# Performance work log

Hardware: AMD Instinct MI355X
Metric: run time of the kernel (lower is better)

Reference implementation:

```python
import jax, jax.numpy as jnp
import numpy as np

B, S, D, H = 2, 2048, 1024, 16
DH = D // H
NEG = -1000000000.0


def setup_inputs() -> dict:
    key = jax.random.key(0)
    ks = jax.random.split(key, 8)
    q = jax.random.normal(ks[0], (B, S, D), dtype=jnp.float32)
    k = jax.random.normal(ks[1], (B, S, D), dtype=jnp.float32)
    v = jax.random.normal(ks[2], (B, S, D), dtype=jnp.float32)
    # padding mask [B, k_len]; ensure first key position is valid
    mask = jax.random.randint(ks[3], (B, S), 0, 2, dtype=jnp.int32)
    mask = mask.at[:, 0].set(1)
    scale = 1.0 / np.sqrt(D)
    Wq = jax.random.normal(ks[4], (D, D), dtype=jnp.float32) * scale
    Wk = jax.random.normal(ks[5], (D, D), dtype=jnp.float32) * scale
    Wv = jax.random.normal(ks[6], (D, D), dtype=jnp.float32) * scale
    Wo = jax.random.normal(ks[7], (D, D), dtype=jnp.float32) * scale
    return {"q": q, "k": k, "v": v, "mask": mask,
            "Wq": Wq, "Wk": Wk, "Wv": Wv, "Wo": Wo}


def reference(q, k, v, mask, Wq, Wk, Wv, Wo):
    # nn.Linear(bias=False): y = x @ W.T  (W is [out, in])
    Q = jnp.einsum('bsd,ed->bse', q, Wq)
    K = jnp.einsum('bsd,ed->bse', k, Wk)
    V = jnp.einsum('bsd,ed->bse', v, Wv)
    # split heads -> [B, H, S, DH]
    Q = Q.reshape(B, S, H, DH).transpose(0, 2, 1, 3)
    K = K.reshape(B, S, H, DH).transpose(0, 2, 1, 3)
    V = V.reshape(B, S, H, DH).transpose(0, 2, 1, 3)
    scores = jnp.einsum('bhqd,bhkd->bhqk', Q, K) / jnp.float32(np.sqrt(DH))
    # padding mask: [B, K] -> additive [B, 1, 1, K]
    pad = jnp.where(mask == 0, jnp.float32(NEG), jnp.float32(0.0))[:, None, None, :]
    scores = scores + pad
    # causal (mask_future=True): strict upper triangle blocked
    causal = jnp.where(jnp.triu(jnp.ones((S, S), dtype=bool), k=1),
                       jnp.float32(NEG), jnp.float32(0.0))
    scores = scores + causal
    attn = jax.nn.softmax(scores, axis=-1)
    out = jnp.einsum('bhqk,bhkd->bhqd', attn, V)  # [B, H, S, DH]
    out = out.transpose(0, 2, 1, 3).reshape(B, S, D)
    out = jnp.einsum('bsd,ed->bse', out, Wo)
    # dropout: identity in eval mode
    return out
```

## Files before the change

### kernel.cpp

```cpp
#include <hip/hip_runtime.h>
#include <stdint.h>

#define BB 2
#define SS 2048
#define DD 1024
#define HH 16
#define DHH 64

typedef __bf16 bf16_t;
typedef bf16_t bf16x8 __attribute__((ext_vector_type(8)));
typedef float f32x4 __attribute__((ext_vector_type(4)));
typedef short s16x4 __attribute__((ext_vector_type(4)));

union FragU { uint4 u; bf16x8 b; };
union Frag4U { uint2 u; s16x4 s; };

#if __has_builtin(__builtin_amdgcn_exp2f)
#define EXP2(x) __builtin_amdgcn_exp2f(x)
#else
#define EXP2(x) exp2f(x)
#endif

__device__ __forceinline__ unsigned short f2bf(float f) {
  union { float f; unsigned int u; } x; x.f = f;
  unsigned int u = x.u;
  return (unsigned short)((u + 0x7FFFu + ((u >> 16) & 1u)) >> 16);
}

__device__ __forceinline__ uint2 pack4(float4 v) {
  uint2 r;
  r.x = (unsigned)f2bf(v.x) | ((unsigned)f2bf(v.y) << 16);
  r.y = (unsigned)f2bf(v.z) | ((unsigned)f2bf(v.w) << 16);
  return r;
}

__device__ __forceinline__ uint2 packAcc(f32x4 a) {
  uint2 r;
  r.x = (unsigned)f2bf(a[0]) | ((unsigned)f2bf(a[1]) << 16);
  r.y = (unsigned)f2bf(a[2]) | ((unsigned)f2bf(a[3]) << 16);
  return r;
}

__device__ __forceinline__ bf16x8 ldsFrag(const unsigned short* s, int idx) {
  FragU f;
  f.u = *reinterpret_cast<const uint4*>(s + idx);
  return f.b;
}

__device__ __forceinline__ void gload_lds16(const unsigned short* g, unsigned short* s) {
  __builtin_amdgcn_global_load_lds(
      (const __attribute__((address_space(1))) unsigned int*)g,
      (__attribute__((address_space(3))) unsigned int*)s, 16, 0, 0);
}

#define MFMA16(a, b, c) __builtin_amdgcn_mfma_f32_16x16x32_bf16((a), (b), (c), 0, 0, 0)
#define MFMA16K16(a, b, c) __builtin_amdgcn_mfma_f32_16x16x16bf16_1k((a), (b), (c), 0, 0, 0)

__global__ __launch_bounds__(256) void convert_kernel(
    const float* __restrict__ q, const float* __restrict__ k, const float* __restrict__ v,
    const float* __restrict__ Wq, const float* __restrict__ Wk,
    const float* __restrict__ Wv, const float* __restrict__ Wo,
    const int* __restrict__ mask,
    unsigned short* __restrict__ Ab, unsigned short* __restrict__ Wb,
    float* __restrict__ Mf) {
  const int z = blockIdx.y;
  if (z == 7) {
    if (blockIdx.x >= 4) return;
    const size_t base = (size_t)blockIdx.x * 1024 + (size_t)threadIdx.x * 4;
    int4 m4 = *reinterpret_cast<const int4*>(mask + base);
    float4 p;
    p.x = (m4.x == 0) ? -1.0e9f : 0.0f;
    p.y = (m4.y == 0) ? -1.0e9f : 0.0f;
    p.z = (m4.z == 0) ? -1.0e9f : 0.0f;
    p.w = (m4.w == 0) ? -1.0e9f : 0.0f;
    *reinterpret_cast<float4*>(Mf + base) = p;
    return;
  }
  const float* src;
  unsigned short* dst;
  float scale = 1.0f;
  if (z < 3) {
    src = (z == 0) ? q : (z == 1) ? k : v;
    dst = Ab + (size_t)z * BB * SS * DD;
  } else {
    if (blockIdx.x >= (DD * DD / 1024)) return;
    src = (z == 3) ? Wq : (z == 4) ? Wk : (z == 5) ? Wv : Wo;
    dst = Wb + (size_t)(z - 3) * DD * DD;
    if (z == 3) scale = 0.125f * 1.44269504088896f;
  }
  const size_t base = (size_t)blockIdx.x * 1024 + (size_t)threadIdx.x * 4;
  float4 val = *reinterpret_cast<const float4*>(src + base);
  val.x *= scale; val.y *= scale; val.z *= scale; val.w *= scale;
  uint2 p = pack4(val);
  *reinterpret_cast<uint2*>(dst + base) = p;
}

__global__ __launch_bounds__(256) void proj128_kernel(
    const unsigned short* __restrict__ Ab, const unsigned short* __restrict__ Wb,
    unsigned short* __restrict__ Qb, unsigned short* __restrict__ Kb,
    unsigned short* __restrict__ Vt) {
  __shared__ unsigned short sA[2][128 * 64];
  __shared__ unsigned short sB[2][128 * 64];

  const int z = blockIdx.z;
  const unsigned short* A = Ab + (size_t)z * BB * SS * DD;
  const unsigned short* W = Wb + (size_t)z * DD * DD;
  unsigned short* Out = (z == 0) ? Qb : (z == 1) ? Kb : Vt;
  const int layout = (z == 2) ? 1 : 0;

  const int t = threadIdx.x;
  const int lane = t & 63, wave = t >> 6;
  const int quad = lane >> 4, l15 = lane & 15;
  const int wr = wave >> 1, wc = wave & 1;
  const int mBase = blockIdx.x * 128, nBase = blockIdx.y * 128;
  const int srow = lane >> 3, soct = lane & 7;

  f32x4 acc[4][4] = {};

  #pragma unroll
  for (int i = 0; i < 4; ++i) {
    const int g = wave * 4 + i;
    const int row = g * 8 + srow;
    const int oct = soct ^ (row & 7);
    gload_lds16(A + (size_t)(mBase + row) * DD + oct * 8, &sA[0][g * 512]);
    gload_lds16(W + (size_t)(nBase + row) * DD + oct * 8, &sB[0][g * 512]);
  }

  for (int kt = 0; kt < DD / 64; ++kt) {
    __syncthreads();
    if (kt + 1 < DD / 64) {
      const int nb = (kt + 1) & 1;
      const int k1 = (kt + 1) * 64;
      #pragma unroll
      for (int i = 0; i < 4; ++i) {
        const int g = wave * 4 + i;
        const int row = g * 8 + srow;
        const int oct = soct ^ (row & 7);
        gload_lds16(A + (size_t)(mBase + row) * DD + k1 + oct * 8, &sA[nb][g * 512]);
        gload_lds16(W + (size_t)(nBase + row) * DD + k1 + oct * 8, &sB[nb][g * 512]);
      }
    }
    const int cb = kt & 1;
    #pragma unroll
    for (int kk = 0; kk < 2; ++kk) {
      bf16x8 af[4], bfr[4];
      #pragma unroll
      for (int i = 0; i < 4; ++i) {
        const int row = wr * 64 + i * 16 + l15;
        af[i] = ldsFrag(sA[cb], (row * 8 + ((kk * 4 + quad) ^ (l15 & 7))) * 8);
      }
      #pragma unroll
      for (int j = 0; j < 4; ++j) {
        const int row = wc * 64 + j * 16 + l15;
        bfr[j] = ldsFrag(sB[cb], (row * 8 + ((kk * 4 + quad) ^ (l15 & 7))) * 8);
      }
      if (layout == 0) {
        #pragma unroll
        for (int i = 0; i < 4; ++i)
          #pragma unroll
          for (int j = 0; j < 4; ++j)
            acc[i][j] = MFMA16(bfr[j], af[i], acc[i][j]);
      } else {
        #pragma unroll
        for (int i = 0; i < 4; ++i)
          #pragma unroll
          for (int j = 0; j < 4; ++j)
            acc[i][j] = MFMA16(af[i], bfr[j], acc[i][j]);
      }
    }
  }

  const int b = mBase >> 11;
  const int sbase = mBase & (SS - 1);
  if (layout == 0) {
    #pragma unroll
    for (int i = 0; i < 4; ++i) {
      #pragma unroll
      for (int j = 0; j < 4; ++j) {
        const int s = sbase + wr * 64 + i * 16 + l15;
        const int n = nBase + wc * 64 + j * 16 + quad * 4;
        const int h = n >> 6, dh = n & (DHH - 1);
        uint2 w = packAcc(acc[i][j]);
        *reinterpret_cast<uint2*>(
            Out + ((size_t)(b * HH + h) * SS + s) * DHH + dh) = w;
      }
    }
  } else {
    #pragma unroll
    for (int i = 0; i < 4; ++i) {
      #pragma unroll
      for (int j = 0; j < 4; ++j) {
        const int s = sbase + wr * 64 + i * 16 + quad * 4;
        const int n = nBase + wc * 64 + j * 16 + l15;
        const int h = n >> 6, dh = n & (DHH - 1);
        uint2 w = packAcc(acc[i][j]);
        *reinterpret_cast<uint2*>(
            Out + ((size_t)(b * HH + h) * DHH + dh) * SS + s) = w;
      }
    }
  }
}

__global__ __launch_bounds__(256, 4) void attn_kernel(
    const unsigned short* __restrict__ Qb, const unsigned short* __restrict__ Kb,
    const unsigned short* __restrict__ Vt, const float* __restrict__ Mf,
    unsigned short* __restrict__ Obh) {
  __shared__ __align__(16) unsigned short sK[2][64 * 64];
  __shared__ __align__(16) unsigned short sV[2][64 * 64];
  __shared__ __align__(16) float sM[SS];
  unsigned short* sO = &sK[0][0];

  const int t = threadIdx.x;
  const int lane = t & 63, wave = t >> 6;
  const int quad = lane >> 4, l15 = lane & 15;

  const int id = blockIdx.x;
  const int xcd = id & 7, rest = id >> 3;
  const int hg = rest >> 5;
  const int hd = xcd * 4 + hg;
  const int r5 = rest & 31;
  const int qt = (hg & 1) ? (31 - r5) : r5;
  const int b = hd >> 4;
  const int qb = qt * 64;

  const size_t headOff = (size_t)hd * SS * DHH;
  const unsigned short* Qh = Qb + headOff;
  const unsigned short* Kh = Kb + headOff;
  const unsigned short* Vh = Vt + headOff;
  const float* Mp = Mf + b * SS;

  bf16x8 aq[2];
  {
    const unsigned short* qp = Qh + (size_t)(qb + wave * 16 + l15) * DHH + quad * 8;
    FragU f0, f1;
    f0.u = *reinterpret_cast<const uint4*>(qp);
    f1.u = *reinterpret_cast<const uint4*>(qp + 32);
    aq[0] = f0.b; aq[1] = f1.b;
  }

  const int srow = lane >> 3, soct = lane & 7;

  #pragma unroll
  for (int i = 0; i < 2; ++i) {
    const int g = wave * 2 + i;
    gload_lds16(reinterpret_cast<const unsigned short*>(Mp + g * 256 + lane * 4),
                reinterpret_cast<unsigned short*>(&sM[g * 256]));
  }

  #pragma unroll
  for (int i = 0; i < 2; ++i) {
    const int g = wave * 2 + i;
    const int row = g * 8 + srow;
    const int oct = soct ^ (row & 7);
    gload_lds16(Kh + (size_t)row * DHH + oct * 8, &sK[0][g * 512]);
    gload_lds16(Vh + (size_t)row * SS + oct * 8, &sV[0][g * 512]);
  }

  float l_lane = 0.0f;
  f32x4 oacc[4] = {};
  const int qrow_abs = qb + wave * 16 + l15;

  for (int c = 0; c <= qt; ++c) {
    __syncthreads();
    if (c < qt) {
      const int c1 = (c + 1) * 64;
      const int nb = (c + 1) & 1;
      #pragma unroll
      for (int i = 0; i < 2; ++i) {
        const int g = wave * 2 + i;
        const int row = g * 8 + srow;
        const int oct = soct ^ (row & 7);
        gload_lds16(Kh + (size_t)(c1 + row) * DHH + oct * 8, &sK[nb][g * 512]);
        gload_lds16(Vh + (size_t)row * SS + c1 + oct * 8, &sV[nb][g * 512]);
      }
    }
    const int cb = c & 1;
    const int c0 = c * 64;

    f32x4 sacc[4] = {};
    #pragma unroll
    for (int kk = 0; kk < 2; ++kk) {
      #pragma unroll
      for (int j = 0; j < 4; ++j) {
        const int row = j * 16 + l15;
        bf16x8 ak = ldsFrag(sK[cb], (row * 8 + ((kk * 4 + quad) ^ (l15 & 7))) * 8);
        sacc[j] = MFMA16(ak, aq[kk], sacc[j]);
      }
    }

    const bool diag = (c == qt);
    s16x4 pk[4];
    #pragma unroll
    for (int j = 0; j < 4; ++j) {
      float4 pf = *reinterpret_cast<const float4*>(&sM[c0 + j * 16 + quad * 4]);
      float p0 = EXP2(sacc[j][0] + pf.x);
      float p1 = EXP2(sacc[j][1] + pf.y);
      float p2 = EXP2(sacc[j][2] + pf.z);
      float p3 = EXP2(sacc[j][3] + pf.w);
      if (diag) {
        const int key = c0 + j * 16 + quad * 4;
        p0 = (key + 0 > qrow_abs) ? 0.0f : p0;
        p1 = (key + 1 > qrow_abs) ? 0.0f : p1;
        p2 = (key + 2 > qrow_abs) ? 0.0f : p2;
        p3 = (key + 3 > qrow_abs) ? 0.0f : p3;
      }
      l_lane += (p0 + p1) + (p2 + p3);
      Frag4U fu;
      fu.u.x = __builtin_amdgcn_perm(__float_as_uint(p1) + 0x8000u,
                                     __float_as_uint(p0) + 0x8000u, 0x07060302u);
      fu.u.y = __builtin_amdgcn_perm(__float_as_uint(p3) + 0x8000u,
                                     __float_as_uint(p2) + 0x8000u, 0x07060302u);
      pk[j] = fu.s;
    }

    #pragma unroll
    for (int j = 0; j < 4; ++j) {
      #pragma unroll
      for (int jn = 0; jn < 4; ++jn) {
        const int row = jn * 16 + l15;
        const int oct = (2 * j + (quad >> 1)) ^ (l15 & 7);
        Frag4U av;
        av.u = *reinterpret_cast<const uint2*>(&sV[cb][(row * 8 + oct) * 8 + (quad & 1) * 4]);
        oacc[jn] = MFMA16K16(av.s, pk[j], oacc[jn]);
      }
    }
  }

  float l_l = l_lane + __shfl_xor(l_lane, 16);
  l_l += __shfl_xor(l_l, 32);
  __syncthreads();
  const float inv = 1.0f / l_l;
  #pragma unroll
  for (int jn = 0; jn < 4; ++jn) {
    uint2 w;
    w.x = (unsigned)f2bf(oacc[jn][0] * inv) | ((unsigned)f2bf(oacc[jn][1] * inv) << 16);
    w.y = (unsigned)f2bf(oacc[jn][2] * inv) | ((unsigned)f2bf(oacc[jn][3] * inv) << 16);
    *reinterpret_cast<uint2*>(&sO[(wave * 16 + l15) * 72 + jn * 16 + quad * 4]) = w;
  }
  __syncthreads();
  {
    const int row = t >> 2, seg = t & 3;
    uint4 u0 = *reinterpret_cast<const uint4*>(&sO[row * 72 + seg * 16]);
    uint4 u1 = *reinterpret_cast<const uint4*>(&sO[row * 72 + seg * 16 + 8]);
    unsigned short* dst = Obh + headOff + (size_t)(qb + row) * DHH + seg * 16;
    *reinterpret_cast<uint4*>(dst) = u0;
    *reinterpret_cast<uint4*>(dst + 8) = u1;
  }
}

__global__ __launch_bounds__(256) void outproj_kernel(
    const unsigned short* __restrict__ Obh, const unsigned short* __restrict__ Wb,
    float* __restrict__ Out) {
  __shared__ unsigned short sA[2][128 * 64];
  __shared__ unsigned short sB[2][128 * 64];

  const unsigned short* W = Wb + (size_t)3 * DD * DD;
  const int t = threadIdx.x;
  const int lane = t & 63, wave = t >> 6;
  const int quad = lane >> 4, l15 = lane & 15;
  const int wr = wave >> 1, wc = wave & 1;
  const int mBase = blockIdx.x * 128, nBase = blockIdx.y * 128;
  const int srow = lane >> 3, soct = lane & 7;

  const int bidx = mBase >> 11;
  const int sloc = mBase & (SS - 1);
  const unsigned short* Abase = Obh + (size_t)bidx * HH * SS * DHH;

  f32x4 acc[4][4] = {};

  #pragma unroll
  for (int i = 0; i < 4; ++i) {
    const int g = wave * 4 + i;
    const int row = g * 8 + srow;
    const int oct = soct ^ (row & 7);
    gload_lds16(Abase + ((size_t)0 * SS + sloc + row) * DHH + oct * 8, &sA[0][g * 512]);
    gload_lds16(W + (size_t)(nBase + row) * DD + oct * 8, &sB[0][g * 512]);
  }

  for (int kt = 0; kt < HH; ++kt) {
    __syncthreads();
    if (kt + 1 < HH) {
      const int nb = (kt + 1) & 1;
      #pragma unroll
      for (int i = 0; i < 4; ++i) {
        const int g = wave * 4 + i;
        const int row = g * 8 + srow;
        const int oct = soct ^ (row & 7);
        gload_lds16(Abase + ((size_t)(kt + 1) * SS + sloc + row) * DHH + oct * 8,
                    &sA[nb][g * 512]);
        gload_lds16(W + (size_t)(nBase + row) * DD + (kt + 1) * 64 + oct * 8,
                    &sB[nb][g * 512]);
      }
    }
    const int cb = kt & 1;
    #pragma unroll
    for (int kk = 0; kk < 2; ++kk) {
      bf16x8 af[4], bfr[4];
      #pragma unroll
      for (int i = 0; i < 4; ++i) {
        const int row = wr * 64 + i * 16 + l15;
        af[i] = ldsFrag(sA[cb], (row * 8 + ((kk * 4 + quad) ^ (l15 & 7))) * 8);
      }
      #pragma unroll
      for (int j = 0; j < 4; ++j) {
        const int row = wc * 64 + j * 16 + l15;
        bfr[j] = ldsFrag(sB[cb], (row * 8 + ((kk * 4 + quad) ^ (l15 & 7))) * 8);
      }
      #pragma unroll
      for (int i = 0; i < 4; ++i)
        #pragma unroll
        for (int j = 0; j < 4; ++j)
          acc[i][j] = MFMA16(bfr[j], af[i], acc[i][j]);
    }
  }

  #pragma unroll
  for (int i = 0; i < 4; ++i) {
    #pragma unroll
    for (int j = 0; j < 4; ++j) {
      const int m = mBase + wr * 64 + i * 16 + l15;
      const int n = nBase + wc * 64 + j * 16 + quad * 4;
      float4 w;
      w.x = acc[i][j][0]; w.y = acc[i][j][1];
      w.z = acc[i][j][2]; w.w = acc[i][j][3];
      *reinterpret_cast<float4*>(Out + (size_t)m * DD + n) = w;
    }
  }
}

extern "C" void kernel_launch(void* const* d_in, const int* in_sizes, int n_in,
                              void* d_out, int out_size, void* d_ws, size_t ws_size,
                              hipStream_t stream) {
  (void)in_sizes; (void)n_in; (void)out_size; (void)ws_size;
  const float* q  = (const float*)d_in[0];
  const float* k  = (const float*)d_in[1];
  const float* v  = (const float*)d_in[2];
  const int* mask = (const int*)d_in[3];
  const float* Wq = (const float*)d_in[4];
  const float* Wk = (const float*)d_in[5];
  const float* Wv = (const float*)d_in[6];
  const float* Wo = (const float*)d_in[7];
  float* out = (float*)d_out;

  const size_t AE = (size_t)BB * SS * DD;
  unsigned short* Ab  = (unsigned short*)d_ws;
  unsigned short* Obh = Ab;
  unsigned short* Wb  = Ab + 3 * AE;
  unsigned short* Qb  = Wb + (size_t)4 * DD * DD;
  unsigned short* Kb  = Qb + AE;
  unsigned short* Vt  = Kb + AE;
  float* Mf = (float*)(Vt + AE);

  convert_kernel<<<dim3(AE / 1024, 8), 256, 0, stream>>>(
      q, k, v, Wq, Wk, Wv, Wo, mask, Ab, Wb, Mf);

  proj128_kernel<<<dim3(BB * SS / 128, DD / 128, 3), 256, 0, stream>>>(
      Ab, Wb, Qb, Kb, Vt);

  attn_kernel<<<dim3(32 * HH * BB), 256, 0, stream>>>(Qb, Kb, Vt, Mf, Obh);

  outproj_kernel<<<dim3(BB * SS / 128, DD / 128), 256, 0, stream>>>(Obh, Wb, out);
}
```

Baseline: 220.1 us.

## Split attention waves across key and query halves with cross-wave reduction

Each wave in the attention kernel now covers 32 queries × 32 keys of every 64×64 chunk instead of 16 queries × all 64 keys. This halves the K and V fragment loads from shared memory per MFMA. Partial outputs and row sums from the two key-half waves are combined at the end through shared memory. The causal-masked diagonal chunk is peeled out of the main loop, and s_setprio is raised around the MFMA phases. The cost is more accumulator registers, possibly lower occupancy, and an extra shared-memory reduction step.

```diff
diff --git a/kernel.cpp b/kernel.cpp
--- a/kernel.cpp
+++ b/kernel.cpp
@@ -205,14 +205,15 @@
     const unsigned short* __restrict__ Qb, const unsigned short* __restrict__ Kb,
     const unsigned short* __restrict__ Vt, const float* __restrict__ Mf,
     unsigned short* __restrict__ Obh) {
-  __shared__ __align__(16) unsigned short sK[2][64 * 64];
-  __shared__ __align__(16) unsigned short sV[2][64 * 64];
+  __shared__ __align__(16) unsigned short sKV[4][64 * 64];
   __shared__ __align__(16) float sM[SS];
-  unsigned short* sO = &sK[0][0];
+  unsigned short* sO = &sKV[0][0];
+  float* pbuf = reinterpret_cast<float*>(&sKV[0][0]);
 
   const int t = threadIdx.x;
   const int lane = t & 63, wave = t >> 6;
   const int quad = lane >> 4, l15 = lane & 15;
+  const int kh = wave >> 1, qh = wave & 1;
 
   const int id = blockIdx.x;
   const int xcd = id & 7, rest = id >> 3;
@@ -229,13 +230,15 @@
   const unsigned short* Vh = Vt + headOff;
   const float* Mp = Mf + b * SS;
 
-  bf16x8 aq[2];
-  {
-    const unsigned short* qp = Qh + (size_t)(qb + wave * 16 + l15) * DHH + quad * 8;
+  bf16x8 aq[2][2];
+  #pragma unroll
+  for (int qt2 = 0; qt2 < 2; ++qt2) {
+    const unsigned short* qp =
+        Qh + (size_t)(qb + qh * 32 + qt2 * 16 + l15) * DHH + quad * 8;
     FragU f0, f1;
     f0.u = *reinterpret_cast<const uint4*>(qp);
     f1.u = *reinterpret_cast<const uint4*>(qp + 32);
-    aq[0] = f0.b; aq[1] = f1.b;
+    aq[qt2][0] = f0.b; aq[qt2][1] = f1.b;
   }
 
   const int srow = lane >> 3, soct = lane & 7;
@@ -252,17 +255,86 @@
     const int g = wave * 2 + i;
     const int row = g * 8 + srow;
     const int oct = soct ^ (row & 7);
-    gload_lds16(Kh + (size_t)row * DHH + oct * 8, &sK[0][g * 512]);
-    gload_lds16(Vh + (size_t)row * SS + oct * 8, &sV[0][g * 512]);
-  }
-
-  float l_lane = 0.0f;
-  f32x4 oacc[4] = {};
-  const int qrow_abs = qb + wave * 16 + l15;
-
-  for (int c = 0; c <= qt; ++c) {
+    gload_lds16(Kh + (size_t)row * DHH + oct * 8, &sKV[0][g * 512]);
+    gload_lds16(Vh + (size_t)row * SS + oct * 8, &sKV[2][g * 512]);
+  }
+
+  float l_lane[2] = {0.0f, 0.0f};
+  f32x4 oacc[4][2] = {};
+  const int qrow0 = qb + qh * 32 + l15;
+  const int qrow1 = qrow0 + 16;
+
+#define CHUNK_BODY(C0, CB, MASKED)                                               \
+  {                                                                              \
+    const unsigned short* sKc = &sKV[CB][0];                                     \
+    const unsigned short* sVc = &sKV[2 + (CB)][0];                               \
+    bf16x8 akf[2][2];                   \
+    _Pragma("unroll")                                                            \
+    for (int kt = 0; kt < 2; ++kt)                                               \
+      _Pragma("unroll")                                                          \
+      for (int kk = 0; kk < 2; ++kk) {                                           \
+        const int row = kh * 32 + kt * 16 + l15;                                 \
+        akf[kt][kk] = ldsFrag(sKc, (row * 8 + ((kk * 4 + quad) ^ (l15 & 7))) * 8); \
+      }                                                                          \
+    f32x4 sacc[2][2] = {};                                        \
+    __builtin_amdgcn_s_setprio(1);                                               \
+    _Pragma("unroll")                                                            \
+    for (int kt = 0; kt < 2; ++kt)                                               \
+      _Pragma("unroll")                                                          \
+      for (int qt2 = 0; qt2 < 2; ++qt2) {                                        \
+        f32x4 tmp = MFMA16(akf[kt][0], aq[qt2][0], sacc[kt][qt2]);               \
+        sacc[kt][qt2] = MFMA16(akf[kt][1], aq[qt2][1], tmp);                     \
+      }                                                                          \
+    __builtin_amdgcn_s_setprio(0);                                               \
+    s16x4 pk[2][2];                                                              \
+    _Pragma("unroll")                                                            \
+    for (int kt = 0; kt < 2; ++kt) {                                             \
+      const int keyb = (C0) + kh * 32 + kt * 16 + quad * 4;                      \
+      float4 pf = *reinterpret_cast<const float4*>(&sM[keyb]);                   \
+      _Pragma("unroll")                                                          \
+      for (int qt2 = 0; qt2 < 2; ++qt2) {                                        \
+        float p0 = EXP2(sacc[kt][qt2][0] + pf.x);                                \
+        float p1 = EXP2(sacc[kt][qt2][1] + pf.y);                                \
+        float p2 = EXP2(sacc[kt][qt2][2] + pf.z);                                \
+        float p3 = EXP2(sacc[kt][qt2][3] + pf.w);                                \
+        if (MASKED) {                                                            \
+          const int qr = qt2 ? qrow1 : qrow0;                                    \
+          p0 = (keyb + 0 > qr) ? 0.0f : p0;                                      \
+          p1 = (keyb + 1 > qr) ? 0.0f : p1;                                      \
+          p2 = (keyb + 2 > qr) ? 0.0f : p2;                                      \
+          p3 = (keyb + 3 > qr) ? 0.0f : p3;                                      \
+        }                                                                        \
+        l_lane[qt2] += (p0 + p1) + (p2 + p3);                                    \
+        Frag4U fu;                                                               \
+        fu.u.x = __builtin_amdgcn_perm(__float_as_uint(p1) + 0x8000u,            \
+                                       __float_as_uint(p0) + 0x8000u,            \
+                                       0x07060302u);                             \
+        fu.u.y = __builtin_amdgcn_perm(__float_as_uint(p3) + 0x8000u,            \
+                                       __float_as_uint(p2) + 0x8000u,            \
+                                       0x07060302u);                             \
+        pk[kt][qt2] = fu.s;                                                      \
+      }                                                                          \
+    }                                                                            \
+    __builtin_amdgcn_s_setprio(1);                                               \
+    _Pragma("unroll")                                                            \
+    for (int kt = 0; kt < 2; ++kt) {                                             \
+      _Pragma("unroll")                                                          \
+      for (int jn = 0; jn < 4; ++jn) {                                           \
+        const int row = jn * 16 + l15;                                           \
+        const int oct = (4 * kh + 2 * kt + (quad >> 1)) ^ (l15 & 7);             \
+        Frag4U av;                                                               \
+        av.u = *reinterpret_cast<const uint2*>(                                  \
+            &sVc[(row * 8 + oct) * 8 + (quad & 1) * 4]);                         \
+        oacc[jn][0] = MFMA16K16(av.s, pk[kt][0], oacc[jn][0]);                   \
+        oacc[jn][1] = MFMA16K16(av.s, pk[kt][1], oacc[jn][1]);                   \
+      }                                                                          \
+    }                                                                            \
+    __builtin_amdgcn_s_setprio(0);                                               \
+  }
+
+  for (int c = 0; c < qt; ++c) {
     __syncthreads();
-    if (c < qt) {
+    {
       const int c1 = (c + 1) * 64;
       const int nb = (c + 1) & 1;
       #pragma unroll
@@ -270,72 +342,64 @@
         const int g = wave * 2 + i;
         const int row = g * 8 + srow;
         const int oct = soct ^ (row & 7);
-        gload_lds16(Kh + (size_t)(c1 + row) * DHH + oct * 8, &sK[nb][g * 512]);
-        gload_lds16(Vh + (size_t)row * SS + c1 + oct * 8, &sV[nb][g * 512]);
-      }
-    }
-    const int cb = c & 1;
-    const int c0 = c * 64;
-
-    f32x4 sacc[4] = {};
-    #pragma unroll
-    for (int kk = 0; kk < 2; ++kk) {
-      #pragma unroll
-      for (int j = 0; j < 4; ++j) {
-        const int row = j * 16 + l15;
-        bf16x8 ak = ldsFrag(sK[cb], (row * 8 + ((kk * 4 + quad) ^ (l15 & 7))) * 8);
-        sacc[j] = MFMA16(ak, aq[kk], sacc[j]);
-      }
-    }
-
-    const bool diag = (c == qt);
-    s16x4 pk[4];
-    #pragma unroll
-    for (int j = 0; j < 4; ++j) {
-      float4 pf = *reinterpret_cast<const float4*>(&sM[c0 + j * 16 + quad * 4]);
-      float p0 = EXP2(sacc[j][0] + pf.x);
-      float p1 = EXP2(sacc[j][1] + pf.y);
-      float p2 = EXP2(sacc[j][2] + pf.z);
-      float p3 = EXP2(sacc[j][3] + pf.w);
-      if (diag) {
-        const int key = c0 + j * 16 + quad * 4;
-        p0 = (key + 0 > qrow_abs) ? 0.0f : p0;
-        p1 = (key + 1 > qrow_abs) ? 0.0f : p1;
-        p2 = (key + 2 > qrow_abs) ? 0.0f : p2;
-        p3 = (key + 3 > qrow_abs) ? 0.0f : p3;
-      }
-      l_lane += (p0 + p1) + (p2 + p3);
-      Frag4U fu;
-      fu.u.x = __builtin_amdgcn_perm(__float_as_uint(p1) + 0x8000u,
-                                     __float_as_uint(p0) + 0x8000u, 0x07060302u);
-      fu.u.y = __builtin_amdgcn_perm(__float_as_uint(p3) + 0x8000u,
-                                     __float_as_uint(p2) + 0x8000u, 0x07060302u);
-      pk[j] = fu.s;
-    }
-
-    #pragma unroll
-    for (int j = 0; j < 4; ++j) {
-      #pragma unroll
-      for (int jn = 0; jn < 4; ++jn) {
-        const int row = jn * 16 + l15;
-        const int oct = (2 * j + (quad >> 1)) ^ (l15 & 7);
-        Frag4U av;
-        av.u = *reinterpret_cast<const uint2*>(&sV[cb][(row * 8 + oct) * 8 + (quad & 1) * 4]);
-        oacc[jn] = MFMA16K16(av.s, pk[j], oacc[jn]);
-      }
-    }
-  }
-
-  float l_l = l_lane + __shfl_xor(l_lane, 16);
-  l_l += __shfl_xor(l_l, 32);
+        gload_lds16(Kh + (size_t)(c1 + row) * DHH + oct * 8, &sKV[nb][g * 512]);
+        gload_lds16(Vh + (size_t)row * SS + c1 + oct * 8, &sKV[2 + nb][g * 512]);
+      }
+    }
+    CHUNK_BODY(c * 64, c & 1, 0)
+  }
+
+  {
+    __syncthreads();
+    CHUNK_BODY(qt * 64, qt & 1, 1)
+  }
+#undef CHUNK_BODY
+
+  float l0 = l_lane[0] + __shfl_xor(l_lane[0], 16);
+  l0 += __shfl_xor(l0, 32);
+  float l1 = l_lane[1] + __shfl_xor(l_lane[1], 16);
+  l1 += __shfl_xor(l1, 32);
+
   __syncthreads();
-  const float inv = 1.0f / l_l;
+  float* lf = sM;
+  if (lane < 16) {
+    lf[wave * 32 + lane] = l0;
+    lf[wave * 32 + 16 + lane] = l1;
+  }
   #pragma unroll
   for (int jn = 0; jn < 4; ++jn) {
-    uint2 w;
-    w.x = (unsigned)f2bf(oacc[jn][0] * inv) | ((unsigned)f2bf(oacc[jn][1] * inv) << 16);
-    w.y = (unsigned)f2bf(oacc[jn][2] * inv) | ((unsigned)f2bf(oacc[jn][3] * inv) << 16);
-    *reinterpret_cast<uint2*>(&sO[(wave * 16 + l15) * 72 + jn * 16 + quad * 4]) = w;
+    #pragma unroll
+    for (int qt2 = 0; qt2 < 2; ++qt2) {
+      const int qq = qh * 32 + qt2 * 16 + l15;
+      float4 w;
+      w.x = oacc[jn][qt2][0]; w.y = oacc[jn][qt2][1];
+      w.z = oacc[jn][qt2][2]; w.w = oacc[jn][qt2][3];
+      *reinterpret_cast<float4*>(&pbuf[kh * 4096 + qq * 64 + jn * 16 + quad * 4]) = w;
+    }
+  }
+  __syncthreads();
+  if (kh == 0) {
+    const float lt0 = l0 + lf[(wave + 2) * 32 + l15];
+    const float lt1 = l1 + lf[(wave + 2) * 32 + 16 + l15];
+    const float inv0 = 1.0f / lt0, inv1 = 1.0f / lt1;
+    #pragma unroll
+    for (int jn = 0; jn < 4; ++jn) {
+      #pragma unroll
+      for (int qt2 = 0; qt2 < 2; ++qt2) {
+        const int qq = qh * 32 + qt2 * 16 + l15;
+        float4 p = *reinterpret_cast<const float4*>(
+            &pbuf[4096 + qq * 64 + jn * 16 + quad * 4]);
+        const float inv = qt2 ? inv1 : inv0;
+        const float o0 = (oacc[jn][qt2][0] + p.x) * inv;
+        const float o1 = (oacc[jn][qt2][1] + p.y) * inv;
+        const float o2 = (oacc[jn][qt2][2] + p.z) * inv;
+        const float o3 = (oacc[jn][qt2][3] + p.w) * inv;
+        uint2 w;
+        w.x = (unsigned)f2bf(o0) | ((unsigned)f2bf(o1) << 16);
+        w.y = (unsigned)f2bf(o2) | ((unsigned)f2bf(o3) << 16);
+        *reinterpret_cast<uint2*>(&sO[qq * 72 + jn * 16 + quad * 4]) = w;
+      }
+    }
   }
   __syncthreads();
   {
```

Result: no change. 216.4 us (-1.7%).
